# Kernel optimization log

Measured on AMD Instinct MI355X. Metric: run time of the kernel, lower is better.

Reference implementation:

```python
import jax, jax.numpy as jnp
import numpy as np

B, T, HD, NH, DS = 4, 1024, 1024, 16, 64
DH = HD // NH


def setup_inputs() -> dict:
    key = jax.random.key(0)
    ks = jax.random.split(key, 12)
    inp = {
        "data": jax.random.normal(ks[0], (B, T, HD), dtype=jnp.float32),
        "scratch_in": jax.random.normal(ks[1], (B, NH, T, DS), dtype=jnp.float32),
        "qkv_w": jax.random.normal(ks[2], (3 * HD, HD), dtype=jnp.float32) * 0.02,
        "qkv_b": jnp.zeros((3 * HD,), dtype=jnp.float32),
        "out_w": jax.random.normal(ks[3], (HD, HD), dtype=jnp.float32) * 0.02,
        "out_b": jnp.zeros((HD,), dtype=jnp.float32),
        "Wq_s": jax.random.normal(ks[4], (NH, DS, DS), dtype=jnp.float32) * 0.02,
        "Wk_s": jax.random.normal(ks[5], (NH, DS, DS), dtype=jnp.float32) * 0.02,
        "Wv_s": jax.random.normal(ks[6], (NH, DS, DS), dtype=jnp.float32) * 0.02,
        "lambda_s": jnp.float32(0.5),  # buffer; > 1e-8 so gate active
        "per_head_scratch_val": jnp.zeros((NH,), dtype=jnp.float32),
    }
    return inp


def reference(data, scratch_in, qkv_w, qkv_b, out_w, out_b, Wq_s, Wk_s, Wv_s, lambda_s, per_head_scratch_val):
    b, t, hd = data.shape
    nh = Wq_s.shape[0]
    dh = hd // nh
    ds = Wq_s.shape[1]

    qkv = data @ qkv_w.T + qkv_b  # [b, t, 3*hd]
    q, k, v = jnp.split(qkv, 3, axis=2)
    Qc = q.reshape(b, t, nh, dh).transpose(0, 2, 1, 3)  # [b, nh, t, dh]
    Kc = k.reshape(b, t, nh, dh).transpose(0, 2, 1, 3)
    Vc = v.reshape(b, t, nh, dh).transpose(0, 2, 1, 3)

    Qs = jnp.einsum('bhts,hsd->bhtd', scratch_in, Wq_s)
    Ks = jnp.einsum('bhts,hsd->bhtd', scratch_in, Wk_s)
    Vs = jnp.einsum('bhts,hsd->bhtd', scratch_in, Wv_s)

    logits_c = jnp.einsum('bhqd,bhkd->bhqk', Qc, Kc) / jnp.sqrt(jnp.float32(dh))
    logits_s = jnp.einsum('bhqd,bhkd->bhqk', Qs, Ks) / jnp.sqrt(jnp.float32(ds))

    lambda_gate = (lambda_s > 1e-8).astype(logits_c.dtype)
    per_head_val = jnp.exp(per_head_scratch_val).reshape(1, nh, 1, 1)
    scratch_delta = (lambda_gate * lambda_s) * per_head_val * logits_s
    unmasked_logits = logits_c + scratch_delta

    delta_logits_rms = jnp.sqrt(jnp.mean(scratch_delta ** 2))
    row_std_ratio = jnp.mean(jnp.std(logits_s, axis=-1, ddof=1) / (jnp.std(logits_c, axis=-1, ddof=1) + 1e-6))

    causal = jnp.tril(jnp.ones((t, t), dtype=jnp.bool_))  # [t, t]
    total_logits = jnp.where(causal[None, None, :, :], unmasked_logits, -jnp.inf)
    attention_weights = jax.nn.softmax(total_logits, axis=-1)  # [b, nh, t, t]

    content_out = jnp.einsum('bhqk,bhkd->bhqd', attention_weights, Vc)
    scratch_out_mid = jnp.einsum('bhqk,bhkd->bhqd', attention_weights, Vs)

    attn_out = content_out.transpose(0, 2, 1, 3).reshape(b, t, hd)
    attn_out = attn_out @ out_w.T + out_b
    return attn_out, scratch_out_mid, delta_logits_rms, row_std_ratio
```

## Files before the change

### kernel.cpp

```cpp
#include <hip/hip_runtime.h>
#include <math.h>
#include <stdint.h>

#define B_ 4
#define T_ 1024
#define NH_ 16
#define MSZ (4194304)

typedef float f4 __attribute__((ext_vector_type(4)));
typedef float f32x4 __attribute__((ext_vector_type(4)));
typedef __bf16 bf16x8 __attribute__((ext_vector_type(8)));
typedef __bf16 bf16x4 __attribute__((ext_vector_type(4)));

static __device__ __forceinline__ f32x4 mfma16(bf16x8 a, bf16x8 b, f32x4 c) {
    return __builtin_amdgcn_mfma_f32_16x16x32_bf16(a, b, c, 0, 0, 0);
}

static __device__ __forceinline__ void gld16(const void* g, void* l) {
    auto gp = reinterpret_cast<const uint32_t __attribute__((address_space(1)))*>(
        reinterpret_cast<uintptr_t>(g));
    auto lp = reinterpret_cast<uint32_t __attribute__((address_space(3)))*>(
        reinterpret_cast<uintptr_t>(l));
    __builtin_amdgcn_global_load_lds(gp, lp, 16, 0, 0);
}

__global__ void k_zero(float* acc) {
    if (threadIdx.x < 2) acc[threadIdx.x] = 0.f;
}

__global__ __launch_bounds__(256) void k_split(
        const float* __restrict__ data, __bf16* __restrict__ dH, __bf16* __restrict__ dL,
        const float* __restrict__ w1,   __bf16* __restrict__ w1H, __bf16* __restrict__ w1L,
        const float* __restrict__ w2,   __bf16* __restrict__ w2H, __bf16* __restrict__ w2L)
{
    const int gsz = gridDim.x * blockDim.x;
    for (size_t i = blockIdx.x * blockDim.x + threadIdx.x; i < 2097152; i += gsz) {
        const float* s; __bf16 *H, *L; size_t off;
        if (i < 1048576)      { s = data; H = dH;  L = dL;  off = i; }
        else if (i < 1835008) { s = w1;   H = w1H; L = w1L; off = i - 1048576; }
        else                  { s = w2;   H = w2H; L = w2L; off = i - 1835008; }
        f4 v = *(const f4*)(s + off*4);
        bf16x4 h, l;
        #pragma unroll
        for (int j = 0; j < 4; ++j) {
            __bf16 hh = (__bf16)v[j];
            h[j] = hh;
            l[j] = (__bf16)(v[j] - (float)hh);
        }
        *(bf16x4*)(H + off*4) = h;
        *(bf16x4*)(L + off*4) = l;
    }
}

template<int MODE>
__global__ __launch_bounds__(256, 2) void k_gemm(
        const __bf16* __restrict__ AH, const __bf16* __restrict__ AL,
        const __bf16* __restrict__ BH, const __bf16* __restrict__ BL,
        const float* __restrict__ bias,
        __bf16* __restrict__ Qb, __bf16* __restrict__ Kb, __bf16* __restrict__ Vtb,
        float* __restrict__ outf)
{
    __shared__ __bf16 sAH[8192];
    __shared__ __bf16 sAL[8192];
    __shared__ __bf16 sBH[8192];
    __shared__ __bf16 sBL[8192];

    const int tid  = threadIdx.x;
    const int lane = tid & 63;
    const int wid  = tid >> 6;
    const int lr   = lane & 15;
    const int lg   = lane >> 4;
    const int wr   = wid >> 1, wc = wid & 1;
    const int m0 = blockIdx.x * 128;
    const int n0 = blockIdx.y * 128;

    f32x4 acc[4][4];
    #pragma unroll
    for (int i = 0; i < 4; ++i)
        #pragma unroll
        for (int j = 0; j < 4; ++j) acc[i][j] = (f32x4){0.f,0.f,0.f,0.f};

    const int rbase = wid * 32;
    const int srow8 = lane >> 3;
    const int schnk = lane & 7;

    for (int k0 = 0; k0 < 1024; k0 += 64) {
        __syncthreads();
        #pragma unroll
        for (int c = 0; c < 4; ++c) {
            int row = rbase + c*8 + srow8;
            size_t sc_ = (size_t)((schnk ^ (row & 7)) << 4);
            size_t dst = (size_t)(rbase + c*8) * 128;
            size_t asrc = (size_t)(n0 + row) * 2048 + (size_t)k0*2 + sc_;
            size_t bsrc = (size_t)(m0 + row) * 2048 + (size_t)k0*2 + sc_;
            gld16((const char*)AH + asrc, (char*)sAH + dst);
            gld16((const char*)AL + asrc, (char*)sAL + dst);
            gld16((const char*)BH + bsrc, (char*)sBH + dst);
            gld16((const char*)BL + bsrc, (char*)sBL + dst);
        }
        __syncthreads();

        #pragma unroll
        for (int kk = 0; kk < 2; ++kk) {
            bf16x8 ah[4], al[4], bh_[4], bl[4];
            #pragma unroll
            for (int rf = 0; rf < 4; ++rf) {
                int row = wr*64 + rf*16 + lr;
                int byte = row*128 + (((kk*4 + lg) ^ (row & 7)) << 4);
                ah[rf] = *(const bf16x8*)((const char*)sAH + byte);
                al[rf] = *(const bf16x8*)((const char*)sAL + byte);
            }
            #pragma unroll
            for (int n = 0; n < 4; ++n) {
                int row = wc*64 + n*16 + lr;
                int byte = row*128 + (((kk*4 + lg) ^ (row & 7)) << 4);
                bh_[n] = *(const bf16x8*)((const char*)sBH + byte);
                bl[n]  = *(const bf16x8*)((const char*)sBL + byte);
            }
            #pragma unroll
            for (int rf = 0; rf < 4; ++rf)
                #pragma unroll
                for (int n = 0; n < 4; ++n) {
                    acc[rf][n] = mfma16(al[rf], bh_[n], acc[rf][n]);
                    acc[rf][n] = mfma16(ah[rf], bl[n],  acc[rf][n]);
                    acc[rf][n] = mfma16(ah[rf], bh_[n], acc[rf][n]);
                }
        }
    }

    #pragma unroll
    for (int n = 0; n < 4; ++n) {
        int col = m0 + wc*64 + n*16 + lr;
        float bb = bias[col];
        #pragma unroll
        for (int rf = 0; rf < 4; ++rf)
            #pragma unroll
            for (int r = 0; r < 4; ++r) {
                float v = acc[rf][n][r] + bb;
                int trow = n0 + wr*64 + rf*16 + lg*4 + r;
                if (MODE == 1) {
                    outf[(size_t)trow*1024 + col] = v;
                } else {
                    int js = col >> 10;
                    int hh = (col >> 6) & 15;
                    int dd = col & 63;
                    int b  = trow >> 10, t = trow & 1023;
                    int bh = b*16 + hh;
                    __bf16 bv = (__bf16)v;
                    if (js == 0)      Qb [((size_t)bh*1024 + t)*64 + dd] = bv;
                    else if (js == 1) Kb [((size_t)bh*1024 + t)*64 + dd] = bv;
                    else              Vtb[((size_t)bh*64 + dd)*1024 + t] = bv;
                }
            }
    }
}

__global__ __launch_bounds__(256) void k_sproj(const float* __restrict__ sin_,
        const float* __restrict__ Wq, const float* __restrict__ Wk, const float* __restrict__ Wv,
        __bf16* __restrict__ Qsb, __bf16* __restrict__ Ksb, __bf16* __restrict__ Vstb)
{
    __shared__ float inT[64*132];
    __shared__ float Wt[64*68];
    const int tid = threadIdx.x;
    const int tx = tid & 15, ty = tid >> 4;
    const int bh = blockIdx.y;
    const int h  = bh & (NH_-1);
    const int t0 = blockIdx.x * 128;
    const size_t base = ((size_t)bh * T_ + t0) * 64;

    #pragma unroll
    for (int l = 0; l < 8; ++l) {
        int fid = l*256 + tid;
        int row = fid >> 4, c4 = fid & 15;
        f4 a = *(const f4*)&sin_[base + (size_t)row*64 + c4*4];
        #pragma unroll
        for (int j = 0; j < 4; ++j) inT[(c4*4+j)*132 + row] = a[j];
    }

    for (int w = 0; w < 3; ++w) {
        const float* Wp = (w == 0) ? Wq : ((w == 1) ? Wk : Wv);
        __syncthreads();
        #pragma unroll
        for (int l = 0; l < 4; ++l) {
            int fid = l*256 + tid;
            int s = fid >> 4, c4 = fid & 15;
            *(f4*)&Wt[s*68 + c4*4] = *(const f4*)&Wp[(size_t)h*4096 + s*64 + c4*4];
        }
        __syncthreads();
        float acc[8][4] = {};
        #pragma unroll 8
        for (int s = 0; s < 64; ++s) {
            f4 w4 = *(const f4*)&Wt[s*68 + tx*4];
            f4 a0 = *(const f4*)&inT[s*132 + ty*8];
            f4 a1 = *(const f4*)&inT[s*132 + ty*8 + 4];
            #pragma unroll
            for (int r = 0; r < 4; ++r)
                #pragma unroll
                for (int j = 0; j < 4; ++j) {
                    acc[r][j]   += a0[r]*w4[j];
                    acc[4+r][j] += a1[r]*w4[j];
                }
        }
        if (w < 2) {
            __bf16* Op = (w == 0) ? Qsb : Ksb;
            #pragma unroll
            for (int r = 0; r < 8; ++r) {
                bf16x4 v;
                #pragma unroll
                for (int j = 0; j < 4; ++j) v[j] = (__bf16)acc[r][j];
                *(bf16x4*)&Op[base + (size_t)(ty*8+r)*64 + tx*4] = v;
            }
        } else {
            #pragma unroll
            for (int r = 0; r < 8; ++r)
                #pragma unroll
                for (int j = 0; j < 4; ++j)
                    Vstb[((size_t)bh*64 + tx*4+j)*1024 + t0 + ty*8 + r] = (__bf16)acc[r][j];
        }
    }
}

__global__ __launch_bounds__(256, 3) void k_attn(
        const __bf16* __restrict__ Qcb, const __bf16* __restrict__ Kcb, const __bf16* __restrict__ Vtb,
        const __bf16* __restrict__ Qsb, const __bf16* __restrict__ Ksb, const __bf16* __restrict__ Vstb,
        const float* __restrict__ lam, const float* __restrict__ phv,
        __bf16* __restrict__ ctxH, __bf16* __restrict__ ctxL,
        float* __restrict__ out2, float* __restrict__ accum)
{
    __shared__ __bf16 sKC[4096];
    __shared__ __bf16 sKS[4096];
    __shared__ __bf16 sVC[4096];
    __shared__ __bf16 sVS[4096];
    __shared__ __bf16 sP [4096];

    const int tid  = threadIdx.x;
    const int lane = tid & 63;
    const int wid  = tid >> 6;
    const int lr   = lane & 15;
    const int lg   = lane >> 4;
    const int bh   = blockIdx.x;
    const int qt   = 15 - blockIdx.y;
    const int h    = bh & (NH_-1);
    const int b    = bh >> 4;
    const int q0   = qt * 64;

    const float lv   = lam[0];
    const float coef = (lv > 1e-8f ? lv : 0.f) * __expf(phv[h]);

    bf16x8 qcf[2], qsf[2];
    {
        int row = q0 + wid*16 + lr;
        size_t qb = ((size_t)bh*1024 + row)*64;
        #pragma unroll
        for (int hf = 0; hf < 2; ++hf) {
            qcf[hf] = *(const bf16x8*)&Qcb[qb + hf*32 + lg*8];
            qsf[hf] = *(const bf16x8*)&Qsb[qb + hf*32 + lg*8];
        }
    }

    f32x4 Oc[4], Os[4];
    #pragma unroll
    for (int n = 0; n < 4; ++n) { Oc[n] = (f32x4){0,0,0,0}; Os[n] = (f32x4){0,0,0,0}; }

    float m4[4], l4[4];
    float sc_s[4] = {}, qq_c[4] = {}, ss_s[4] = {}, qq_s[4] = {};
    #pragma unroll
    for (int i = 0; i < 4; ++i) { m4[i] = -INFINITY; l4[i] = 0.f; }

    const char* kcB = (const char*)Kcb  + (size_t)bh*1024*128;
    const char* ksB = (const char*)Ksb  + (size_t)bh*1024*128;
    const char* vtB = (const char*)Vtb  + (size_t)bh*64*2048;
    const char* vsB = (const char*)Vstb + (size_t)bh*64*2048;

    for (int kt = 0; kt < 16; ++kt) {
        const bool pv = (kt <= qt);
        __syncthreads();
        #pragma unroll
        for (int c = 0; c < 2; ++c) {
            int trow = wid*16 + c*8 + (lane>>3);
            int sc_  = (lane&7) ^ (trow&7);
            size_t dsto = (size_t)wid*2048 + c*1024;
            gld16(kcB + ((size_t)(kt*64 + trow))*128 + sc_*16, (char*)sKC + dsto);
            gld16(ksB + ((size_t)(kt*64 + trow))*128 + sc_*16, (char*)sKS + dsto);
            if (pv) {
                gld16(vtB + (size_t)trow*2048 + kt*128 + sc_*16, (char*)sVC + dsto);
                gld16(vsB + (size_t)trow*2048 + kt*128 + sc_*16, (char*)sVS + dsto);
            }
        }
        __syncthreads();

        float L[4][4];
        #pragma unroll
        for (int n = 0; n < 4; ++n) {
            int krow = n*16 + lr;
            int rswz = krow & 7;
            const char* pc = (const char*)sKC + krow*128;
            const char* ps = (const char*)sKS + krow*128;
            bf16x8 kc0 = *(const bf16x8*)(pc + (((lg  ) ^ rswz)<<4));
            bf16x8 kc1 = *(const bf16x8*)(pc + (((lg+4) ^ rswz)<<4));
            bf16x8 ks0 = *(const bf16x8*)(ps + (((lg  ) ^ rswz)<<4));
            bf16x8 ks1 = *(const bf16x8*)(ps + (((lg+4) ^ rswz)<<4));
            f32x4 z = {0.f,0.f,0.f,0.f};
            f32x4 sc = mfma16(qcf[1], kc1, mfma16(qcf[0], kc0, z));
            f32x4 ss = mfma16(qsf[1], ks1, mfma16(qsf[0], ks0, z));
            #pragma unroll
            for (int r = 0; r < 4; ++r) {
                sc_s[r] += sc[r];
                qq_c[r] = fmaf(sc[r], sc[r], qq_c[r]);
                ss_s[r] += ss[r];
                qq_s[r] = fmaf(ss[r], ss[r], qq_s[r]);
                L[n][r] = 0.125f * fmaf(coef, ss[r], sc[r]);
            }
        }
        if (!pv) continue;

        if (kt == qt) {
            #pragma unroll
            for (int n = 0; n < 4; ++n) {
                int kc = n*16 + lr;
                #pragma unroll
                for (int r = 0; r < 4; ++r)
                    if (kc > wid*16 + lg*4 + r) L[n][r] = -INFINITY;
            }
        }

        float fr4[4];
        #pragma unroll
        for (int r = 0; r < 4; ++r) {
            float v = fmaxf(fmaxf(L[0][r], L[1][r]), fmaxf(L[2][r], L[3][r]));
            v = fmaxf(v, __shfl_xor(v, 1));
            v = fmaxf(v, __shfl_xor(v, 2));
            v = fmaxf(v, __shfl_xor(v, 4));
            v = fmaxf(v, __shfl_xor(v, 8));
            float mn = fmaxf(m4[r], v);
            float fr = __expf(m4[r] - mn);
            m4[r] = mn; fr4[r] = fr;
            float ps = 0.f;
            #pragma unroll
            for (int n = 0; n < 4; ++n) {
                float p = __expf(L[n][r] - mn);
                L[n][r] = p;
                ps += p;
            }
            l4[r] = l4[r]*fr + ps;
        }
        #pragma unroll
        for (int n = 0; n < 4; ++n)
            #pragma unroll
            for (int r = 0; r < 4; ++r) {
                Oc[n][r] *= fr4[r];
                Os[n][r] *= fr4[r];
            }

        #pragma unroll
        for (int n = 0; n < 4; ++n)
            #pragma unroll
            for (int r = 0; r < 4; ++r) {
                int prow = wid*16 + lg*4 + r;
                *((__bf16*)((char*)sP + prow*128 + ((((n*16+lr)>>3) ^ (prow&7))<<4) + (((n*16+lr)&7)<<1))) = (__bf16)L[n][r];
            }

        bf16x8 pa[2];
        {
            int prow = wid*16 + lr;
            const char* pp = (const char*)sP + prow*128;
            pa[0] = *(const bf16x8*)(pp + (((lg  ) ^ (prow&7))<<4));
            pa[1] = *(const bf16x8*)(pp + (((lg+4) ^ (prow&7))<<4));
        }
        #pragma unroll
        for (int n = 0; n < 4; ++n) {
            int vrow = n*16 + lr;
            int rswz = vrow & 7;
            const char* pc = (const char*)sVC + vrow*128;
            const char* ps = (const char*)sVS + vrow*128;
            bf16x8 vc0 = *(const bf16x8*)(pc + (((lg  ) ^ rswz)<<4));
            bf16x8 vc1 = *(const bf16x8*)(pc + (((lg+4) ^ rswz)<<4));
            bf16x8 vs0 = *(const bf16x8*)(ps + (((lg  ) ^ rswz)<<4));
            bf16x8 vs1 = *(const bf16x8*)(ps + (((lg+4) ^ rswz)<<4));
            Oc[n] = mfma16(pa[1], vc1, mfma16(pa[0], vc0, Oc[n]));
            Os[n] = mfma16(pa[1], vs1, mfma16(pa[0], vs0, Os[n]));
        }
    }

    float d2p = qq_s[0] + qq_s[1] + qq_s[2] + qq_s[3];

    #pragma unroll
    for (int r = 0; r < 4; ++r) {
        #pragma unroll
        for (int msk = 1; msk <= 8; msk <<= 1) {
            l4[r]   += __shfl_xor(l4[r],   msk);
            sc_s[r] += __shfl_xor(sc_s[r], msk);
            qq_c[r] += __shfl_xor(qq_c[r], msk);
            ss_s[r] += __shfl_xor(ss_s[r], msk);
            qq_s[r] += __shfl_xor(qq_s[r], msk);
        }
    }

    #pragma unroll
    for (int r = 0; r < 4; ++r) {
        float linv = 1.0f / l4[r];
        int row = q0 + wid*16 + lg*4 + r;
        #pragma unroll
        for (int n = 0; n < 4; ++n) {
            int d = n*16 + lr;
            float oc = Oc[n][r] * linv;
            size_t cidx = (((size_t)b*T_ + row)*NH_ + h)*64 + d;
            __bf16 hv = (__bf16)oc;
            ctxH[cidx] = hv;
            ctxL[cidx] = (__bf16)(oc - (float)hv);
            out2[((size_t)bh*T_ + row)*64 + d] = Os[n][r] * linv;
        }
    }

    float rp = 0.f;
    #pragma unroll
    for (int r = 0; r < 4; ++r) {
        float S1c = 0.125f    * sc_s[r];
        float S2c = 0.015625f * qq_c[r];
        float S1s = 0.125f    * ss_s[r];
        float S2s = 0.015625f * qq_s[r];
        float varc = (S2c - S1c*S1c*(1.f/1024.f)) * (1.f/1023.f);
        float vars = (S2s - S1s*S1s*(1.f/1024.f)) * (1.f/1023.f);
        rp += sqrtf(fmaxf(vars, 0.f)) / (sqrtf(fmaxf(varc, 0.f)) + 1e-6f);
    }
    rp *= (1.f/16.f);

    #pragma unroll
    for (int msk = 1; msk <= 32; msk <<= 1) {
        d2p += __shfl_xor(d2p, msk);
        rp  += __shfl_xor(rp,  msk);
    }
    __syncthreads();
    float* sred = (float*)sP;
    if (lane == 0) { sred[wid] = d2p; sred[4+wid] = rp; }
    __syncthreads();
    if (tid == 0) {
        float td2 = (sred[0]+sred[1]+sred[2]+sred[3]) * coef * coef * 0.015625f;
        float tr  =  sred[4]+sred[5]+sred[6]+sred[7];
        atomicAdd(&accum[0], td2);
        atomicAdd(&accum[1], tr);
    }
}

__global__ void k_fin(const float* __restrict__ acc, float* __restrict__ out) {
    if (threadIdx.x == 0) {
        out[0] = sqrtf(acc[0] * (1.f/67108864.f));
        out[1] = acc[1] * (1.f/65536.f);
    }
}

extern "C" void kernel_launch(void* const* d_in, const int* in_sizes, int n_in,
                              void* d_out, int out_size, void* d_ws, size_t ws_size,
                              hipStream_t stream)
{
    const float* data  = (const float*)d_in[0];
    const float* sin_  = (const float*)d_in[1];
    const float* qkv_w = (const float*)d_in[2];
    const float* qkv_b = (const float*)d_in[3];
    const float* out_w = (const float*)d_in[4];
    const float* out_b = (const float*)d_in[5];
    const float* Wq    = (const float*)d_in[6];
    const float* Wk    = (const float*)d_in[7];
    const float* Wv    = (const float*)d_in[8];
    const float* lam   = (const float*)d_in[9];
    const float* phv   = (const float*)d_in[10];
    float* out = (float*)d_out;
    char*  w   = (char*)d_ws;

    const size_t MB = 1024*1024;
    __bf16* Qcb   = (__bf16*)(w);
    __bf16* Kcb   = (__bf16*)(w + 8*MB);
    __bf16* Vtb   = (__bf16*)(w + 16*MB);
    __bf16* Qsb   = (__bf16*)(w + 24*MB);
    __bf16* Ksb   = (__bf16*)(w + 32*MB);
    __bf16* Vstb  = (__bf16*)(w + 40*MB);
    __bf16* dataH = (__bf16*)(w + 48*MB);
    __bf16* dataL = (__bf16*)(w + 56*MB);
    __bf16* wH    = (__bf16*)(w + 64*MB);
    __bf16* wL    = (__bf16*)(w + 70*MB);
    __bf16* owH   = (__bf16*)(w + 76*MB);
    __bf16* owL   = (__bf16*)(w + 78*MB);
    float*  accum = (float*)(w + 80*MB);

    k_zero   <<<1, 64, 0, stream>>>(accum);
    k_split  <<<2048, 256, 0, stream>>>(data, dataH, dataL, qkv_w, wH, wL, out_w, owH, owL);
    k_gemm<0><<<dim3(24, 32), 256, 0, stream>>>(dataH, dataL, wH, wL, qkv_b, Qcb, Kcb, Vtb, nullptr);
    k_sproj  <<<dim3(8, 64), 256, 0, stream>>>(sin_, Wq, Wk, Wv, Qsb, Ksb, Vstb);
    k_attn   <<<dim3(64, 16), 256, 0, stream>>>(Qcb, Kcb, Vtb, Qsb, Ksb, Vstb, lam, phv,
                                                dataH, dataL, out + (size_t)MSZ, accum);
    k_gemm<1><<<dim3(8, 32), 256, 0, stream>>>(dataH, dataL, owH, owL, out_b, nullptr, nullptr, nullptr, out);
    k_fin    <<<1, 64, 0, stream>>>(accum, out + 2*(size_t)MSZ);
}
```

Measured before the change: 357.8 us.

## Double-buffer K/V tiles in attention kernel to overlap loads with compute

Adds double-buffered LDS tiles for content/scratch K and V and issues the next tile's async global-to-LDS loads before computing on the current tile, with a single barrier per iteration. This is meant to hide global memory latency behind the MFMA and softmax work. It doubles LDS for K/V (about 72KB per block), and the launch bound drops from 3 to 2 blocks per CU, which lowers occupancy. Nothing waits on the async loads before the barrier beyond what __syncthreads provides, so ordering relies on the compiler inserting vmcnt waits.

```diff
diff --git a/kernel.cpp b/kernel.cpp
--- a/kernel.cpp
+++ b/kernel.cpp
@@ -220,17 +220,17 @@
     }
 }
 
-__global__ __launch_bounds__(256, 3) void k_attn(
+__global__ __launch_bounds__(256, 2) void k_attn(
         const __bf16* __restrict__ Qcb, const __bf16* __restrict__ Kcb, const __bf16* __restrict__ Vtb,
         const __bf16* __restrict__ Qsb, const __bf16* __restrict__ Ksb, const __bf16* __restrict__ Vstb,
         const float* __restrict__ lam, const float* __restrict__ phv,
         __bf16* __restrict__ ctxH, __bf16* __restrict__ ctxL,
         float* __restrict__ out2, float* __restrict__ accum)
 {
-    __shared__ __bf16 sKC[4096];
-    __shared__ __bf16 sKS[4096];
-    __shared__ __bf16 sVC[4096];
-    __shared__ __bf16 sVS[4096];
+    __shared__ __bf16 sKC[2][4096];
+    __shared__ __bf16 sKS[2][4096];
+    __shared__ __bf16 sVC[2][4096];
+    __shared__ __bf16 sVS[2][4096];
     __shared__ __bf16 sP [4096];
 
     const int tid  = threadIdx.x;
@@ -247,6 +247,30 @@
     const float lv   = lam[0];
     const float coef = (lv > 1e-8f ? lv : 0.f) * __expf(phv[h]);
 
+    const char* kcB = (const char*)Kcb  + (size_t)bh*1024*128;
+    const char* ksB = (const char*)Ksb  + (size_t)bh*1024*128;
+    const char* vtB = (const char*)Vtb  + (size_t)bh*64*2048;
+    const char* vsB = (const char*)Vstb + (size_t)bh*64*2048;
+
+    const int strow0 = wid*16 + (lane>>3);
+    const size_t dsto0 = (size_t)wid*2048;
+
+    auto STAGE = [&](int kt, int buf) {
+        const bool pvn = (kt <= qt);
+        #pragma unroll
+        for (int c = 0; c < 2; ++c) {
+            int trow = strow0 + c*8;
+            int sc_  = (lane&7) ^ (trow&7);
+            size_t dsto = dsto0 + c*1024;
+            gld16(kcB + ((size_t)(kt*64 + trow))*128 + sc_*16, (char*)sKC[buf] + dsto);
+            gld16(ksB + ((size_t)(kt*64 + trow))*128 + sc_*16, (char*)sKS[buf] + dsto);
+            if (pvn) {
+                gld16(vtB + (size_t)trow*2048 + kt*128 + sc_*16, (char*)sVC[buf] + dsto);
+                gld16(vsB + (size_t)trow*2048 + kt*128 + sc_*16, (char*)sVS[buf] + dsto);
+            }
+        }
+    };
+
     bf16x8 qcf[2], qsf[2];
     {
         int row = q0 + wid*16 + lr;
@@ -267,35 +291,21 @@
     #pragma unroll
     for (int i = 0; i < 4; ++i) { m4[i] = -INFINITY; l4[i] = 0.f; }
 
-    const char* kcB = (const char*)Kcb  + (size_t)bh*1024*128;
-    const char* ksB = (const char*)Ksb  + (size_t)bh*1024*128;
-    const char* vtB = (const char*)Vtb  + (size_t)bh*64*2048;
-    const char* vsB = (const char*)Vstb + (size_t)bh*64*2048;
-
+    STAGE(0, 0);
+    __syncthreads();
+
+    int cur = 0;
     for (int kt = 0; kt < 16; ++kt) {
         const bool pv = (kt <= qt);
-        __syncthreads();
-        #pragma unroll
-        for (int c = 0; c < 2; ++c) {
-            int trow = wid*16 + c*8 + (lane>>3);
-            int sc_  = (lane&7) ^ (trow&7);
-            size_t dsto = (size_t)wid*2048 + c*1024;
-            gld16(kcB + ((size_t)(kt*64 + trow))*128 + sc_*16, (char*)sKC + dsto);
-            gld16(ksB + ((size_t)(kt*64 + trow))*128 + sc_*16, (char*)sKS + dsto);
-            if (pv) {
-                gld16(vtB + (size_t)trow*2048 + kt*128 + sc_*16, (char*)sVC + dsto);
-                gld16(vsB + (size_t)trow*2048 + kt*128 + sc_*16, (char*)sVS + dsto);
-            }
-        }
-        __syncthreads();
+        if (kt < 15) STAGE(kt + 1, cur ^ 1);
 
         float L[4][4];
         #pragma unroll
         for (int n = 0; n < 4; ++n) {
             int krow = n*16 + lr;
             int rswz = krow & 7;
-            const char* pc = (const char*)sKC + krow*128;
-            const char* ps = (const char*)sKS + krow*128;
+            const char* pc = (const char*)sKC[cur] + krow*128;
+            const char* ps = (const char*)sKS[cur] + krow*128;
             bf16x8 kc0 = *(const bf16x8*)(pc + (((lg  ) ^ rswz)<<4));
             bf16x8 kc1 = *(const bf16x8*)(pc + (((lg+4) ^ rswz)<<4));
             bf16x8 ks0 = *(const bf16x8*)(ps + (((lg  ) ^ rswz)<<4));
@@ -312,74 +322,78 @@
                 L[n][r] = 0.125f * fmaf(coef, ss[r], sc[r]);
             }
         }
-        if (!pv) continue;
-
-        if (kt == qt) {
+
+        if (pv) {
+            if (kt == qt) {
+                #pragma unroll
+                for (int n = 0; n < 4; ++n) {
+                    int kc = n*16 + lr;
+                    #pragma unroll
+                    for (int r = 0; r < 4; ++r)
+                        if (kc > wid*16 + lg*4 + r) L[n][r] = -INFINITY;
+                }
+            }
+
+            float fr4[4];
+            #pragma unroll
+            for (int r = 0; r < 4; ++r) {
+                float v = fmaxf(fmaxf(L[0][r], L[1][r]), fmaxf(L[2][r], L[3][r]));
+                v = fmaxf(v, __shfl_xor(v, 1));
+                v = fmaxf(v, __shfl_xor(v, 2));
+                v = fmaxf(v, __shfl_xor(v, 4));
+                v = fmaxf(v, __shfl_xor(v, 8));
+                float mn = fmaxf(m4[r], v);
+                float fr = __expf(m4[r] - mn);
+                m4[r] = mn; fr4[r] = fr;
+                float ps = 0.f;
+                #pragma unroll
+                for (int n = 0; n < 4; ++n) {
+                    float p = __expf(L[n][r] - mn);
+                    L[n][r] = p;
+                    ps += p;
+                }
+                l4[r] = l4[r]*fr + ps;
+            }
+            #pragma unroll
+            for (int n = 0; n < 4; ++n)
+                #pragma unroll
+                for (int r = 0; r < 4; ++r) {
+                    Oc[n][r] *= fr4[r];
+                    Os[n][r] *= fr4[r];
+                }
+
+            #pragma unroll
+            for (int n = 0; n < 4; ++n)
+                #pragma unroll
+                for (int r = 0; r < 4; ++r) {
+                    int prow = wid*16 + lg*4 + r;
+                    *((__bf16*)((char*)sP + prow*128 + ((((n*16+lr)>>3) ^ (prow&7))<<4) + (((n*16+lr)&7)<<1))) = (__bf16)L[n][r];
+                }
+
+            bf16x8 pa[2];
+            {
+                int prow = wid*16 + lr;
+                const char* pp = (const char*)sP + prow*128;
+                pa[0] = *(const bf16x8*)(pp + (((lg  ) ^ (prow&7))<<4));
+                pa[1] = *(const bf16x8*)(pp + (((lg+4) ^ (prow&7))<<4));
+            }
             #pragma unroll
             for (int n = 0; n < 4; ++n) {
-                int kc = n*16 + lr;
-                #pragma unroll
-                for (int r = 0; r < 4; ++r)
-                    if (kc > wid*16 + lg*4 + r) L[n][r] = -INFINITY;
-            }
-        }
-
-        float fr4[4];
-        #pragma unroll
-        for (int r = 0; r < 4; ++r) {
-            float v = fmaxf(fmaxf(L[0][r], L[1][r]), fmaxf(L[2][r], L[3][r]));
-            v = fmaxf(v, __shfl_xor(v, 1));
-            v = fmaxf(v, __shfl_xor(v, 2));
-            v = fmaxf(v, __shfl_xor(v, 4));
-            v = fmaxf(v, __shfl_xor(v, 8));
-            float mn = fmaxf(m4[r], v);
-            float fr = __expf(m4[r] - mn);
-            m4[r] = mn; fr4[r] = fr;
-            float ps = 0.f;
-            #pragma unroll
-            for (int n = 0; n < 4; ++n) {
-                float p = __expf(L[n][r] - mn);
-                L[n][r] = p;
-                ps += p;
-            }
-            l4[r] = l4[r]*fr + ps;
-        }
-        #pragma unroll
-        for (int n = 0; n < 4; ++n)
-            #pragma unroll
-            for (int r = 0; r < 4; ++r) {
-                Oc[n][r] *= fr4[r];
-                Os[n][r] *= fr4[r];
-            }
-
-        #pragma unroll
-        for (int n = 0; n < 4; ++n)
-            #pragma unroll
-            for (int r = 0; r < 4; ++r) {
-                int prow = wid*16 + lg*4 + r;
-                *((__bf16*)((char*)sP + prow*128 + ((((n*16+lr)>>3) ^ (prow&7))<<4) + (((n*16+lr)&7)<<1))) = (__bf16)L[n][r];
-            }
-
-        bf16x8 pa[2];
-        {
-            int prow = wid*16 + lr;
-            const char* pp = (const char*)sP + prow*128;
-            pa[0] = *(const bf16x8*)(pp + (((lg  ) ^ (prow&7))<<4));
-            pa[1] = *(const bf16x8*)(pp + (((lg+4) ^ (prow&7))<<4));
-        }
-        #pragma unroll
-        for (int n = 0; n < 4; ++n) {
-            int vrow = n*16 + lr;
-            int rswz = vrow & 7;
-            const char* pc = (const char*)sVC + vrow*128;
-            const char* ps = (const char*)sVS + vrow*128;
-            bf16x8 vc0 = *(const bf16x8*)(pc + (((lg  ) ^ rswz)<<4));
-            bf16x8 vc1 = *(const bf16x8*)(pc + (((lg+4) ^ rswz)<<4));
-            bf16x8 vs0 = *(const bf16x8*)(ps + (((lg  ) ^ rswz)<<4));
-            bf16x8 vs1 = *(const bf16x8*)(ps + (((lg+4) ^ rswz)<<4));
-            Oc[n] = mfma16(pa[1], vc1, mfma16(pa[0], vc0, Oc[n]));
-            Os[n] = mfma16(pa[1], vs1, mfma16(pa[0], vs0, Os[n]));
-        }
+                int vrow = n*16 + lr;
+                int rswz = vrow & 7;
+                const char* pc = (const char*)sVC[cur] + vrow*128;
+                const char* ps = (const char*)sVS[cur] + vrow*128;
+                bf16x8 vc0 = *(const bf16x8*)(pc + (((lg  ) ^ rswz)<<4));
+                bf16x8 vc1 = *(const bf16x8*)(pc + (((lg+4) ^ rswz)<<4));
+                bf16x8 vs0 = *(const bf16x8*)(ps + (((lg  ) ^ rswz)<<4));
+                bf16x8 vs1 = *(const bf16x8*)(ps + (((lg+4) ^ rswz)<<4));
+                Oc[n] = mfma16(pa[1], vc1, mfma16(pa[0], vc0, Oc[n]));
+                Os[n] = mfma16(pa[1], vs1, mfma16(pa[0], vs0, Os[n]));
+            }
+        }
+
+        __syncthreads();
+        cur ^= 1;
     }
 
     float d2p = qq_s[0] + qq_s[1] + qq_s[2] + qq_s[3];
```

Measured after the change: 329.2 us. 8.0% less time.
